# Kernel tuning notes

Measured on AMD Instinct MI355X. Metric: run time of the kernel, lower is better.

## Reference

```python
import jax, jax.numpy as jnp
import numpy as np

BS, CH, T = 128, 16, 12288
RED = 6          # mini_window_temporal_reduction_factor
N = CH * RED     # 96 mini-windows
K = 5            # top-k selected mini-windows
NCLS = 5
LATENT = (T // 16) * 8  # hypernet flatten dim = 6144


def _conv1d(x, w, b=None):
    # x: [B,C,L], w: [O,I,ks] -> [B,O,L-ks+1]
    out = jax.lax.conv_general_dilated(x, w, (1,), 'VALID', dimension_numbers=('NCH', 'OIH', 'NCH'))
    return out if b is None else out + b[None, :, None]


def _same_reflect(x, w, b):
    p = (w.shape[-1] - 1) // 2
    return _conv1d(jnp.pad(x, ((0, 0), (0, 0), (p, p)), mode='reflect'), w, b)


def _leaky(z):
    return jnp.where(z >= 0, z, 0.01 * z)


def _pool(x, f, op):
    L = x.shape[-1] // f  # floor, drop remainder (matches torch pooling)
    xr = x[..., :L * f].reshape(x.shape[:-1] + (L, f))
    return op(xr, -1)


def setup_inputs() -> dict:
    key = jax.random.key(0)
    ks = jax.random.split(key, 18)
    s = 0.05
    return {
        'x': jax.random.normal(ks[0], (BS, CH, T), jnp.float32),
        'epoch': 0,
        # hypernet conv blocks (padding='same', reflect)
        'hw1': jax.random.normal(ks[1], (32, CH, 7), jnp.float32) * s,
        'hb1': jnp.zeros((32,), jnp.float32),
        'hw2': jax.random.normal(ks[2], (64, 32, 7), jnp.float32) * s,
        'hb2': jnp.zeros((64,), jnp.float32),
        'hw3': jax.random.normal(ks[3], (8, 64, 7), jnp.float32) * s,
        'hb3': jnp.zeros((8,), jnp.float32),
        'hl1': jax.random.normal(ks[4], (N, LATENT), jnp.float32) * s,  # Linear(latent->N), no bias
        'hl2': jax.random.normal(ks[5], (N, N), jnp.float32) * s,       # Linear(N->N), no bias
        # GroupedIdxConv1D: per-group Conv1d(1, 64, ks=15); bias only for group 0
        'gw': jax.random.normal(ks[6], (CH, 64, 15), jnp.float32) * s,
        'gb0': jax.random.normal(ks[7], (64,), jnp.float32) * s,
        # encoder convs 1,2
        'ew2': jax.random.normal(ks[8], (128, 64, 7), jnp.float32) * s,
        'eb2': jnp.zeros((128,), jnp.float32),
        'ew3': jax.random.normal(ks[9], (128, 128, 7), jnp.float32) * s,
        'eb3': jnp.zeros((128,), jnp.float32),
        # classifier
        'cw': jax.random.normal(ks[10], (NCLS, 128), jnp.float32) * s,
        'cb': jnp.zeros((NCLS,), jnp.float32),
    }


def reference(x, epoch, hw1, hb1, hw2, hb2, hw3, hb3, hl1, hl2, gw, gb0, ew2, eb2, ew3, eb3, cw, cb):
    # Eval-mode forward (active sampling, no Gumbel noise, hard top-k one-hot, dropout off)
    bs = x.shape[0]
    # ---- hypernet ----
    h = _pool(_leaky(_same_reflect(x, hw1, hb1)), 4, jnp.mean)
    h = _pool(_leaky(_same_reflect(h, hw2, hb2)), 4, jnp.mean)
    h = jnp.tanh(_same_reflect(h, hw3, hb3)).reshape(bs, -1)
    logits = _leaky(h @ hl1.T) @ hl2.T  # [bs, N]
    # ---- hard top-k sampling (bmm with one-hot == gather rows) ----
    _, idx = jax.lax.top_k(logits, K)                      # [bs, K]
    x_r = x.reshape(bs, N, -1)                             # [bs, N, T']
    sel = jnp.take_along_axis(x_r, idx[:, :, None], axis=1)  # [bs, K, T']
    gidx = idx // RED                                      # ExG channel group per mini-window
    # ---- GroupedIdxConv1D: per-element kernel gather + conv + sum over K ----
    ksz = gw.shape[-1]
    Lout = sel.shape[-1] - ksz + 1
    windows = jnp.stack([sel[..., i:i + Lout] for i in range(ksz)], axis=-1)  # [bs,K,Lout,ksz]
    kernels = gw[gidx]                                     # [bs,K,64,ksz]
    z = jnp.einsum('bkls,bkos->bol', windows, kernels)     # conv + sum over channel axis K
    n0 = (gidx == 0).sum(1).astype(z.dtype)                # bias only for group 0 elements
    z = z + n0[:, None, None] * gb0[None, :, None]
    # ---- encoder tail ----
    z = _pool(_leaky(z), 4, jnp.max)
    z = _pool(_leaky(_conv1d(z, ew2, eb2)), 4, jnp.max)
    z = _conv1d(z, ew3, eb3).mean(-1)                      # AdaptiveAvgPool1d(1) -> [bs,128]
    # ---- classifier ----
    return jax.nn.log_softmax(z @ cw.T + cb, -1)           # [bs, NCLS]
```

## Files before the change

### kernel.cpp

```cpp
#include <hip/hip_runtime.h>
#include <hip/hip_bf16.h>
#include <math.h>

typedef unsigned short u16;
typedef __attribute__((ext_vector_type(8))) short short8;
typedef __attribute__((ext_vector_type(4))) float floatx4;

__device__ __forceinline__ float lk(float v){ return v >= 0.f ? v : 0.01f*v; }
__device__ __forceinline__ u16 f2b(float f){
    __hip_bfloat16 h = __float2bfloat16(f);
    return *reinterpret_cast<u16*>(&h);
}
__device__ __forceinline__ int refl(int t, int L){
    return t < 0 ? -t : (t >= L ? 2*L-2-t : t);
}

__global__ __launch_bounds__(256) void k_prep(const float* __restrict__ hw1,
        const float* __restrict__ hw2, const float* __restrict__ ew2,
        const float* __restrict__ gw, const float* __restrict__ ew3,
        u16* __restrict__ wb, float* __restrict__ wt)
{
    int idx = blockIdx.x*256 + threadIdx.x;
    if (idx < 4096){
        int u = idx; int j=u&7; int o=(u>>3)&31; int kq=(u>>8)&3; int s=u>>10;
        int tap = 2*s + (kq>>1); int ic = (kq&1)*8 + j;
        wb[idx] = (tap<7) ? f2b(hw1[(o*16+ic)*7+tap]) : (u16)0;
    } else if (idx < 18432){
        int u = idx - 4096; int j=u&7; int o=(u>>3)&63; int kq=(u>>9)&3; int s=u>>11;
        wb[idx] = f2b(hw2[(o*32 + kq*8 + j)*7 + s]);
    } else if (idx < 75776){
        int u = idx - 18432; int j=u&7; int o=(u>>3)&127; int kq=(u>>10)&3; int s=u>>12;
        int ih = s/7, tap = s-ih*7;
        wb[idx] = f2b(ew2[(o*64 + ih*32 + kq*8 + j)*7 + tap]);
    } else if (idx < 92160){
        int u = idx - 75776; int j=u&7; int o=(u>>3)&63; int tb=(u>>9)&1; int gi=u>>10;
        int tap = tb*8 + j;
        wb[idx] = (tap<15) ? f2b(gw[gi*960 + o*15 + tap]) : (u16)0;
    } else if (idx < 206848){
        int u = idx - 92160;
        int o = u & 127; int ic = (u >> 7) & 127; int tap = u >> 14;
        wt[u] = ew3[((size_t)o*128 + ic)*7 + tap];
    }
}

__global__ __launch_bounds__(256,4) void k_hconv1(const float* __restrict__ x,
        const u16* __restrict__ wb1, const float* __restrict__ bias,
        u16* __restrict__ h1)
{
    __shared__ __align__(16) u16 xs[2][264*24];
    __shared__ __align__(16) u16 ob[2][64*32];
    int b = blockIdx.x >> 3, chunk = blockIdx.x & 7;
    int tid = threadIdx.x;
    const float* xb = x + (size_t)b*16*12288;
    int wv = tid >> 6, lane = tid & 63;
    int m = lane & 15, kq = lane >> 4;
    int tq = wv;

    short8 wfr[4][2];
    #pragma unroll
    for (int s=0;s<4;s++)
        #pragma unroll
        for (int oh=0;oh<2;oh++)
            wfr[s][oh] = *reinterpret_cast<const short8*>(
                            &wb1[(((s*4+kq)*32) + oh*16 + m)*8]);
    float bv[2] = { bias[m], bias[16+m] };

    float rg0[16]; float rgx;
    int exrow = 256 + (tid>>4), exch = tid & 15;

#define LOADTILE(G0) { \
        int t0 = refl((G0) - 3 + tid, 12288); \
        _Pragma("unroll") \
        for (int ic=0;ic<16;ic++) rg0[ic] = xb[(size_t)ic*12288 + t0]; \
        if (tid < 128){ \
            int t1 = refl((G0) - 3 + exrow, 12288); \
            rgx = xb[(size_t)exch*12288 + t1]; \
        } \
        __builtin_amdgcn_sched_barrier(0); }

#define WRITETILE(BUF) { \
        short8 p0, p1; \
        _Pragma("unroll") \
        for (int j=0;j<8;j++){ p0[j] = (short)f2b(rg0[j]); p1[j] = (short)f2b(rg0[8+j]); } \
        *reinterpret_cast<short8*>(&xs[BUF][tid*24])     = p0; \
        *reinterpret_cast<short8*>(&xs[BUF][tid*24 + 8]) = p1; \
        if (tid < 128) xs[BUF][exrow*24 + exch] = f2b(rgx); }

#define COMPUTETILE(BUF) { \
        floatx4 acc[4][2]; \
        _Pragma("unroll") \
        for (int i=0;i<4;i++){ acc[i][0] = (floatx4){0.f,0.f,0.f,0.f}; \
                               acc[i][1] = (floatx4){0.f,0.f,0.f,0.f}; } \
        _Pragma("unroll") \
        for (int sub=0; sub<4; sub++){ \
            int tb = tq*64 + sub*16; \
            _Pragma("unroll") \
            for (int s=0;s<4;s++){ \
                int tap = 2*s + (kq>>1); \
                short8 xfr = *reinterpret_cast<const short8*>( \
                                &xs[BUF][(tb + m + tap)*24 + (kq&1)*8]); \
                acc[sub][0] = __builtin_amdgcn_mfma_f32_16x16x32_bf16(xfr, wfr[s][0], acc[sub][0], 0,0,0); \
                acc[sub][1] = __builtin_amdgcn_mfma_f32_16x16x32_bf16(xfr, wfr[s][1], acc[sub][1], 0,0,0); \
            } \
        } \
        _Pragma("unroll") \
        for (int sub=0; sub<4; sub++){ \
            int p = tq*16 + sub*4 + kq; \
            _Pragma("unroll") \
            for (int oh=0; oh<2; oh++){ \
                float sum = lk(acc[sub][oh][0]+bv[oh]) + lk(acc[sub][oh][1]+bv[oh]) \
                          + lk(acc[sub][oh][2]+bv[oh]) + lk(acc[sub][oh][3]+bv[oh]); \
                ob[BUF][p*32 + oh*16 + m] = f2b(sum*0.25f); \
            } \
        } }

#define STORETILE(BUF, TAU) { \
        short8 v = *reinterpret_cast<const short8*>(&ob[BUF][tid*8]); \
        *reinterpret_cast<short8*>(&h1[((size_t)b*3072 + (TAU)*64)*32 + tid*8]) = v; }

    int tau0 = chunk*6;
    LOADTILE(tau0*256);
    WRITETILE(0);
    __syncthreads();
    LOADTILE((tau0+1)*256);
    #pragma unroll 1
    for (int t=0; t<6; ++t){
        int cur = t & 1;
        COMPUTETILE(cur);
        if (t < 5) WRITETILE(cur^1);
        __syncthreads();
        STORETILE(cur, tau0 + t);
        if (t < 4) LOADTILE((tau0 + t + 2)*256);
    }

#undef LOADTILE
#undef WRITETILE
#undef COMPUTETILE
#undef STORETILE
}

__global__ __launch_bounds__(256,3) void k_hconv2(const u16* __restrict__ h1,
        const u16* __restrict__ wb2, const float* __restrict__ bias,
        float* __restrict__ h2)
{
    __shared__ __align__(16) u16 xs[2][198*40];
    int b = blockIdx.x >> 3, tile = blockIdx.x & 7;
    int tid = threadIdx.x;
    int wv = tid >> 6, lane = tid & 63;
    int m = lane & 15, kq = lane >> 4;

    float bv[4];
    #pragma unroll
    for (int nt=0;nt<4;nt++) bv[nt] = bias[nt*16 + m];

    short8 rgA[3], rgX;

#define LOADH(HALF) { \
        int gh = tile*384 + (HALF)*192 - 3; \
        _Pragma("unroll") \
        for (int cc=0;cc<3;cc++){ \
            int c = tid + cc*256; \
            int row = c >> 2, q = c & 3; \
            int t = refl(gh + row, 3072); \
            rgA[cc] = *reinterpret_cast<const short8*>(&h1[((size_t)b*3072 + t)*32 + q*8]); \
        } \
        if (tid < 24){ \
            int c = 768 + tid; \
            int row = c >> 2, q = c & 3; \
            int t = refl(gh + row, 3072); \
            rgX = *reinterpret_cast<const short8*>(&h1[((size_t)b*3072 + t)*32 + q*8]); \
        } \
        __builtin_amdgcn_sched_barrier(0); }

#define WRITEH(BUF) { \
        _Pragma("unroll") \
        for (int cc=0;cc<3;cc++){ \
            int c = tid + cc*256; \
            *reinterpret_cast<short8*>(&xs[BUF][(c>>2)*40 + (c&3)*8]) = rgA[cc]; \
        } \
        if (tid < 24){ \
            int c = 768 + tid; \
            *reinterpret_cast<short8*>(&xs[BUF][(c>>2)*40 + (c&3)*8]) = rgX; \
        } }

#define COMPUTEH(BUF, HALF) { \
        floatx4 acc[3][4]; \
        _Pragma("unroll") \
        for (int i=0;i<3;i++) \
            _Pragma("unroll") \
            for (int nt=0;nt<4;nt++) acc[i][nt] = (floatx4){0.f,0.f,0.f,0.f}; \
        _Pragma("unroll") \
        for (int nt2=0; nt2<2; ++nt2){ \
            short8 wfr[7][2]; \
            _Pragma("unroll") \
            for (int s=0;s<7;s++) \
                _Pragma("unroll") \
                for (int c=0;c<2;c++) \
                    wfr[s][c] = *reinterpret_cast<const short8*>( \
                        &wb2[(((s*4+kq)*64) + (nt2*2+c)*16 + m)*8]); \
            _Pragma("unroll") \
            for (int i=0;i<3;i++){ \
                int tb = (wv*3+i)*16; \
                _Pragma("unroll") \
                for (int s=0;s<7;s++){ \
                    short8 xfr = *reinterpret_cast<const short8*>( \
                                    &xs[BUF][(tb + m + s)*40 + kq*8]); \
                    acc[i][nt2*2]   = __builtin_amdgcn_mfma_f32_16x16x32_bf16(xfr, wfr[s][0], acc[i][nt2*2],   0,0,0); \
                    acc[i][nt2*2+1] = __builtin_amdgcn_mfma_f32_16x16x32_bf16(xfr, wfr[s][1], acc[i][nt2*2+1], 0,0,0); \
                } \
            } \
        } \
        _Pragma("unroll") \
        for (int i=0;i<3;i++){ \
            int pooled = (wv*3+i)*4 + kq; \
            _Pragma("unroll") \
            for (int nt=0;nt<4;nt++){ \
                float sum = lk(acc[i][nt][0]+bv[nt]) + lk(acc[i][nt][1]+bv[nt]) \
                          + lk(acc[i][nt][2]+bv[nt]) + lk(acc[i][nt][3]+bv[nt]); \
                h2[((size_t)b*768 + tile*96 + (HALF)*48 + pooled)*64 + nt*16 + m] = sum*0.25f; \
            } \
        } }

    LOADH(0);
    WRITEH(0);
    __syncthreads();
    LOADH(1);
    COMPUTEH(0, 0);
    WRITEH(1);
    __syncthreads();
    COMPUTEH(1, 1);

#undef LOADH
#undef WRITEH
#undef COMPUTEH
}

__global__ __launch_bounds__(256) void k_hconv3(const float* __restrict__ h2,
        const float* __restrict__ w, const float* __restrict__ bias,
        float* __restrict__ latent)
{
    __shared__ float xs[64*201];
    int b = blockIdx.x >> 2, tile = blockIdx.x & 3;
    int g0 = tile*192;
    int tid = threadIdx.x;
    for (int idx = tid; idx < 198*64; idx += 256){
        int jj = idx >> 6, ic = idx & 63;
        int t = refl(g0 + jj - 3, 768);
        xs[ic*201 + jj] = h2[((size_t)b*768 + t)*64 + ic];
    }
    __syncthreads();
    int c = tid >> 5, run = tid & 31;
    int p0 = run*6;
    float acc[6];
    #pragma unroll
    for (int l=0;l<6;l++) acc[l] = 0.f;
    for (int ic=0; ic<64; ic++){
        const float* wp = w + (c*64+ic)*7;
        float wr[7];
        #pragma unroll
        for (int s=0;s<7;s++) wr[s] = wp[s];
        const float* xr = xs + ic*201 + p0;
        float xw[12];
        #pragma unroll
        for (int j=0;j<12;j++) xw[j] = xr[j];
        #pragma unroll
        for (int s=0;s<7;s++)
            #pragma unroll
            for (int l=0;l<6;l++) acc[l] += wr[s]*xw[l+s];
    }
    float bv = bias[c];
    float* op = latent + (size_t)b*6144 + c*768 + g0 + p0;
    #pragma unroll
    for (int l=0;l<6;l++) op[l] = tanhf(acc[l] + bv);
}

__global__ __launch_bounds__(256) void k_lin1(const float* __restrict__ latent,
        const float* __restrict__ hl1, float* __restrict__ t1)
{
    __shared__ float ls[6144];
    int b = blockIdx.x / 6, ntile = blockIdx.x % 6;
    int tid = threadIdx.x;
    const float4* lp = reinterpret_cast<const float4*>(latent + (size_t)b*6144);
    float4* lsv = reinterpret_cast<float4*>(ls);
    for (int i = tid; i < 1536; i += 256) lsv[i] = lp[i];
    __syncthreads();
    int wv = tid >> 6, lane = tid & 63;
    #pragma unroll
    for (int nn=0; nn<4; nn++){
        int n = ntile*16 + wv*4 + nn;
        const float4* wp = reinterpret_cast<const float4*>(hl1 + (size_t)n*6144);
        float s = 0.f;
        #pragma unroll
        for (int j=0;j<24;j++){
            float4 q = wp[lane + 64*j];
            float4 l4 = lsv[lane + 64*j];
            s += l4.x*q.x + l4.y*q.y + l4.z*q.z + l4.w*q.w;
        }
        #pragma unroll
        for (int off=32; off; off>>=1) s += __shfl_down(s, off);
        if (lane==0) t1[b*96+n] = lk(s);
    }
}

__global__ __launch_bounds__(128) void k_topk(const float* __restrict__ t1,
        const float* __restrict__ hl2, int* __restrict__ idxb, float* __restrict__ n0f)
{
    __shared__ float lg[96];
    int b = blockIdx.x, n = threadIdx.x;
    if (n < 96){
        float s = 0.f;
        const float* tp = t1 + b*96;
        const float* wp = hl2 + n*96;
        for (int m=0;m<96;m++) s += tp[m]*wp[m];
        lg[n] = s;
    }
    __syncthreads();
    if (threadIdx.x == 0){
        unsigned long long u0=0ull, u1=0ull;
        float n0 = 0.f;
        for (int k=0;k<5;k++){
            float best = -3.4e38f; int bi = 0;
            for (int m=0;m<96;m++){
                bool used = m<64 ? ((u0>>m)&1ull) : ((u1>>(m-64))&1ull);
                if (!used && lg[m] > best){ best = lg[m]; bi = m; }
            }
            if (bi<64) u0 |= 1ull<<bi; else u1 |= 1ull<<(bi-64);
            idxb[b*5+k] = bi;
            if (bi < 6) n0 += 1.f;
        }
        n0f[b] = n0;
    }
}

__global__ __launch_bounds__(256,3) void k_gconv(const float* __restrict__ x,
        const int* __restrict__ idxb, const float* __restrict__ n0f,
        const u16* __restrict__ gwb, const float* __restrict__ gb0,
        u16* __restrict__ zp)
{
    __shared__ __align__(16) u16 xs[5][8][536];
    __shared__ int nidx[5];
    __shared__ float n0s;
    int b = blockIdx.x >> 2, qc = blockIdx.x & 3;
    int tid = threadIdx.x;
    int p0g = qc*512;

    if (tid < 5) nidx[tid] = idxb[b*5 + tid];
    if (tid == 5) n0s = n0f[b];
    __syncthreads();

    for (int cch = tid; cch < 5*134; cch += 256){
        int k = cch / 134, q = cch - k*134;
        const float* xrow = x + (size_t)b*196608 + (size_t)nidx[k]*2048;
        int base = p0g + q*4;
        u16 vb[4];
        if (base + 3 <= 2047){
            float4 a = *reinterpret_cast<const float4*>(xrow + base);
            vb[0]=f2b(a.x); vb[1]=f2b(a.y); vb[2]=f2b(a.z); vb[3]=f2b(a.w);
        } else {
            #pragma unroll
            for (int jj=0;jj<4;jj++){
                int ii = base+jj; if (ii > 2047) ii = 2047;
                vb[jj] = f2b(xrow[ii]);
            }
        }
        #pragma unroll
        for (int jj=0;jj<4;jj++){
            int gof = q*4 + jj;
            #pragma unroll
            for (int r=0;r<8;r++){
                int i = gof - r;
                if (i >= 0 && i < 528) xs[k][r][i] = vb[jj];
            }
        }
    }

    int wv = tid >> 6, lane = tid & 63;
    int m = lane & 15, kq = lane >> 4;
    int o = wv*16 + m;

    short8 wfr[3];
    #pragma unroll
    for (int c=0;c<3;c++){
        int kk = 2*c + (kq>>1);
        int kkc = kk < 5 ? kk : 4;
        int gi = nidx[kkc] / 6;
        short8 f = *reinterpret_cast<const short8*>(
                        &gwb[(((gi*2 + (kq&1))*64)+o)*8]);
        if (kk >= 5) f = (short8)(short)0;
        wfr[c] = f;
    }
    float bv = n0s * gb0[o];
    __syncthreads();

    int rr = m & 7, ibase = (m & 8) + (kq & 1)*8;
    for (int g8 = 0; g8 < 4; ++g8){
        floatx4 acc[8];
        #pragma unroll
        for (int i=0;i<8;i++) acc[i] = (floatx4){0.f,0.f,0.f,0.f};
        #pragma unroll
        for (int s8=0; s8<8; ++s8){
            int P = (g8*8 + s8)*16;
            #pragma unroll
            for (int c=0;c<3;c++){
                int kk = 2*c + (kq>>1);
                int kkc = kk < 5 ? kk : 4;
                short8 af = *reinterpret_cast<const short8*>(&xs[kkc][rr][P + ibase]);
                acc[s8] = __builtin_amdgcn_mfma_f32_16x16x32_bf16(af, wfr[c], acc[s8], 0,0,0);
            }
        }
        #pragma unroll
        for (int s8=0; s8<8; ++s8){
            int sub = g8*8 + s8;
            int Q = qc*128 + sub*4 + kq;
            if (Q < 508){
                float mx = fmaxf(fmaxf(lk(acc[s8][0]+bv), lk(acc[s8][1]+bv)),
                                 fmaxf(lk(acc[s8][2]+bv), lk(acc[s8][3]+bv)));
                zp[((size_t)b*508 + Q)*64 + o] = f2b(mx);
            }
        }
    }
}

__global__ __launch_bounds__(256,2) void k_econv2(const u16* __restrict__ zp,
        const u16* __restrict__ wbe, const float* __restrict__ bias,
        float* __restrict__ p2)
{
    __shared__ __align__(16) u16 xs[134*72];
    int b = blockIdx.x >> 2, tile = blockIdx.x & 3;
    int tid = threadIdx.x;
    int r0 = tile*128;
    for (int c = tid; c < 134*8; c += 256){
        int row = c >> 3, q = c & 7;
        int t = r0 + row; if (t > 507) t = 507;
        *reinterpret_cast<short8*>(&xs[row*72 + q*8]) =
            *reinterpret_cast<const short8*>(&zp[((size_t)b*508 + t)*64 + q*8]);
    }
    int wv = tid >> 6, lane = tid & 63;
    int m = lane & 15, kq = lane >> 4;

    short8 wfr[2][14];
    #pragma unroll
    for (int h=0;h<2;h++){
        int o = (wv + 4*h)*16 + m;
        #pragma unroll
        for (int s=0;s<14;s++)
            wfr[h][s] = *reinterpret_cast<const short8*>(&wbe[(((s*4+kq)*128)+o)*8]);
    }
    float bv[2] = { bias[wv*16 + m], bias[(wv+4)*16 + m] };
    __syncthreads();

    for (int sub=0; sub<8; sub++){
        floatx4 acc[2];
        acc[0] = (floatx4){0.f,0.f,0.f,0.f};
        acc[1] = (floatx4){0.f,0.f,0.f,0.f};
        #pragma unroll
        for (int s=0;s<14;s++){
            int tap = s%7, ih = s/7;
            short8 xfr = *reinterpret_cast<const short8*>(
                            &xs[(sub*16 + m + tap)*72 + ih*32 + kq*8]);
            acc[0] = __builtin_amdgcn_mfma_f32_16x16x32_bf16(xfr, wfr[0][s], acc[0], 0,0,0);
            acc[1] = __builtin_amdgcn_mfma_f32_16x16x32_bf16(xfr, wfr[1][s], acc[1], 0,0,0);
        }
        int pg = tile*32 + sub*4 + kq;
        if (pg < 125){
            #pragma unroll
            for (int h=0;h<2;h++){
                float mx = fmaxf(fmaxf(lk(acc[h][0]+bv[h]), lk(acc[h][1]+bv[h])),
                                 fmaxf(lk(acc[h][2]+bv[h]), lk(acc[h][3]+bv[h])));
                p2[((size_t)b*125 + pg)*128 + (wv+4*h)*16 + m] = mx;
            }
        }
    }
}

__global__ __launch_bounds__(128) void k_tail(const float* __restrict__ p2,
        const float* __restrict__ wt, const float* __restrict__ bias,
        const float* __restrict__ cw, const float* __restrict__ cb,
        float* __restrict__ out)
{
    __shared__ float ss[7][128];
    __shared__ float ft[128];
    __shared__ float lgs[5];
    int b = blockIdx.x, tid = threadIdx.x;

    {
        const float* pb = p2 + (size_t)b*125*128 + tid;
        float first6[6], last6[6];
        float c = 0.f;
        #pragma unroll
        for (int t=0;t<6;t++){ float v = pb[(size_t)t*128]; first6[t]=v; c+=v; }
        for (int t=6;t<119;t++) c += pb[(size_t)t*128];
        #pragma unroll
        for (int t=0;t<6;t++) last6[t] = pb[(size_t)(119+t)*128];
        ss[0][tid] = c;
        #pragma unroll
        for (int s=0;s<6;s++){ c = c - first6[s] + last6[s]; ss[s+1][tid] = c; }
    }
    __syncthreads();

    {
        const float* ssl = &ss[0][0];
        float s = 0.f;
        #pragma unroll 8
        for (int u=0; u<896; u++)
            s += wt[(size_t)u*128 + tid] * ssl[u];
        ft[tid] = s*(1.f/119.f) + bias[tid];
    }
    __syncthreads();

    if (tid < 5){
        float lg = cb[tid];
        const float* wp = cw + tid*128;
        for (int o=0;o<128;o++) lg += ft[o]*wp[o];
        lgs[tid] = lg;
    }
    __syncthreads();
    if (tid == 0){
        float mx = -3.4e38f;
        for (int c=0;c<5;c++) mx = fmaxf(mx, lgs[c]);
        float se = 0.f;
        for (int c=0;c<5;c++) se += expf(lgs[c]-mx);
        float lse = mx + logf(se);
        for (int c=0;c<5;c++) out[b*5+c] = lgs[c]-lse;
    }
}

extern "C" void kernel_launch(void* const* d_in, const int* in_sizes, int n_in,
                              void* d_out, int out_size, void* d_ws, size_t ws_size,
                              hipStream_t stream)
{
    const float* x   = (const float*)d_in[0];
    const float* hw1 = (const float*)d_in[2];
    const float* hb1 = (const float*)d_in[3];
    const float* hw2 = (const float*)d_in[4];
    const float* hb2 = (const float*)d_in[5];
    const float* hw3 = (const float*)d_in[6];
    const float* hb3 = (const float*)d_in[7];
    const float* hl1 = (const float*)d_in[8];
    const float* hl2 = (const float*)d_in[9];
    const float* gw  = (const float*)d_in[10];
    const float* gb0 = (const float*)d_in[11];
    const float* ew2 = (const float*)d_in[12];
    const float* eb2 = (const float*)d_in[13];
    const float* ew3 = (const float*)d_in[14];
    const float* eb3 = (const float*)d_in[15];
    const float* cw  = (const float*)d_in[16];
    const float* cb  = (const float*)d_in[17];
    float* out = (float*)d_out;

    float* f       = (float*)d_ws;
    float* latent  = f;
    float* t1      = f + 786432;
    int*   idxb    = (int*)(f + 806432);
    float* n0f     = f + 808432;
    u16*   zpb     = (u16*)(f + 810000);
    u16*   wb      = (u16*)(f + 2900000);
    float* h2      = f + 3932160;
    float* p2      = f + 7100000;
    u16*   h1b     = (u16*)(f + 10223616);
    float* wt      = f + 16600000;

    k_prep<<<808, 256, 0, stream>>>(hw1, hw2, ew2, gw, ew3, wb, wt);
    k_hconv1<<<1024, 256, 0, stream>>>(x, wb, hb1, h1b);
    k_hconv2<<<1024, 256, 0, stream>>>(h1b, wb + 4096, hb2, h2);
    k_hconv3<<<512, 256, 0, stream>>>(h2, hw3, hb3, latent);
    k_lin1<<<768, 256, 0, stream>>>(latent, hl1, t1);
    k_topk<<<128, 128, 0, stream>>>(t1, hl2, idxb, n0f);
    k_gconv<<<512, 256, 0, stream>>>(x, idxb, n0f, wb + 75776, gb0, zpb);
    k_econv2<<<512, 256, 0, stream>>>(zpb, wb + 18432, eb2, p2);
    k_tail<<<128, 128, 0, stream>>>(p2, wt, eb3, cw, cb, out);
}
```

Measured before the change: 356.5 us.

## Fuse linear layers and top-k into one per-batch kernel; raise hconv2 occupancy

Merges the first hypernet linear layer, the second linear layer and the top-k selection into a single kernel with one block per batch element, keeping intermediate activations in shared memory. This removes one launch and a global round-trip for t1. It also raises the minimum-blocks hint for the second hypernet conv to 4. The trade-off is far fewer blocks (128 vs 768) for the large weight-reading GEMV, so each wave does six times more serial work, and the tighter register budget in hconv2 may cause spills.

```diff
diff --git a/kernel.cpp b/kernel.cpp
--- a/kernel.cpp
+++ b/kernel.cpp
@@ -139,7 +139,7 @@
 #undef STORETILE
 }
 
-__global__ __launch_bounds__(256,3) void k_hconv2(const u16* __restrict__ h1,
+__global__ __launch_bounds__(256,4) void k_hconv2(const u16* __restrict__ h1,
         const u16* __restrict__ wb2, const float* __restrict__ bias,
         float* __restrict__ h2)
 {
@@ -274,20 +274,21 @@
     for (int l=0;l<6;l++) op[l] = tanhf(acc[l] + bv);
 }
 
-__global__ __launch_bounds__(256) void k_lin1(const float* __restrict__ latent,
-        const float* __restrict__ hl1, float* __restrict__ t1)
+__global__ __launch_bounds__(256) void k_lin(const float* __restrict__ latent,
+        const float* __restrict__ hl1, const float* __restrict__ hl2,
+        int* __restrict__ idxb, float* __restrict__ n0f)
 {
     __shared__ float ls[6144];
-    int b = blockIdx.x / 6, ntile = blockIdx.x % 6;
-    int tid = threadIdx.x;
+    __shared__ float t1s[96];
+    __shared__ float lg[96];
+    int b = blockIdx.x, tid = threadIdx.x;
     const float4* lp = reinterpret_cast<const float4*>(latent + (size_t)b*6144);
     float4* lsv = reinterpret_cast<float4*>(ls);
     for (int i = tid; i < 1536; i += 256) lsv[i] = lp[i];
     __syncthreads();
     int wv = tid >> 6, lane = tid & 63;
-    #pragma unroll
-    for (int nn=0; nn<4; nn++){
-        int n = ntile*16 + wv*4 + nn;
+    for (int nn=0; nn<24; nn++){
+        int n = wv*24 + nn;
         const float4* wp = reinterpret_cast<const float4*>(hl1 + (size_t)n*6144);
         float s = 0.f;
         #pragma unroll
@@ -298,24 +299,17 @@
         }
         #pragma unroll
         for (int off=32; off; off>>=1) s += __shfl_down(s, off);
-        if (lane==0) t1[b*96+n] = lk(s);
-    }
-}
-
-__global__ __launch_bounds__(128) void k_topk(const float* __restrict__ t1,
-        const float* __restrict__ hl2, int* __restrict__ idxb, float* __restrict__ n0f)
-{
-    __shared__ float lg[96];
-    int b = blockIdx.x, n = threadIdx.x;
-    if (n < 96){
+        if (lane==0) t1s[n] = lk(s);
+    }
+    __syncthreads();
+    if (tid < 96){
         float s = 0.f;
-        const float* tp = t1 + b*96;
-        const float* wp = hl2 + n*96;
-        for (int m=0;m<96;m++) s += tp[m]*wp[m];
-        lg[n] = s;
-    }
-    __syncthreads();
-    if (threadIdx.x == 0){
+        const float* wp = hl2 + tid*96;
+        for (int m=0;m<96;m++) s += t1s[m]*wp[m];
+        lg[tid] = s;
+    }
+    __syncthreads();
+    if (tid == 0){
         unsigned long long u0=0ull, u1=0ull;
         float n0 = 0.f;
         for (int k=0;k<5;k++){
@@ -550,7 +544,6 @@
 
     float* f       = (float*)d_ws;
     float* latent  = f;
-    float* t1      = f + 786432;
     int*   idxb    = (int*)(f + 806432);
     float* n0f     = f + 808432;
     u16*   zpb     = (u16*)(f + 810000);
@@ -564,8 +557,7 @@
     k_hconv1<<<1024, 256, 0, stream>>>(x, wb, hb1, h1b);
     k_hconv2<<<1024, 256, 0, stream>>>(h1b, wb + 4096, hb2, h2);
     k_hconv3<<<512, 256, 0, stream>>>(h2, hw3, hb3, latent);
-    k_lin1<<<768, 256, 0, stream>>>(latent, hl1, t1);
-    k_topk<<<128, 128, 0, stream>>>(t1, hl2, idxb, n0f);
+    k_lin<<<128, 256, 0, stream>>>(latent, hl1, hl2, idxb, n0f);
     k_gconv<<<512, 256, 0, stream>>>(x, idxb, n0f, wb + 75776, gb0, zpb);
     k_econv2<<<512, 256, 0, stream>>>(zpb, wb + 18432, eb2, p2);
     k_tail<<<128, 128, 0, stream>>>(p2, wt, eb3, cw, cb, out);
```

After: 574.8 us. 61.2% more time.
